# Kernel optimization log

Hardware: AMD Instinct MI355X
Metric: run time of the kernel (lower is better)

Reference implementation:

```python
import jax, jax.numpy as jnp
import numpy as np

B, NP, N, C, H = 16, 512, 1024, 1024, 16
HD = C // H
HID = 4 * C
EPS = 1e-5


def _layernorm(x, g, b):
    mu = jnp.mean(x, axis=-1, keepdims=True)
    var = jnp.mean(jnp.square(x - mu), axis=-1, keepdims=True)
    return (x - mu) * jax.lax.rsqrt(var + EPS) * g + b


def setup_inputs() -> dict:
    key = jax.random.key(0)
    ks = jax.random.split(key, 12)
    x = jax.random.normal(ks[0], (B, NP, C), dtype=jnp.float32)
    cache_k = jax.random.normal(ks[1], (B, H, N, HD), dtype=jnp.float32)
    cache_v = jax.random.normal(ks[2], (B, H, N, HD), dtype=jnp.float32)
    # update_mask: exactly NP active (to-be-updated) token slots per batch row
    scores = jax.random.uniform(ks[3], (B, N))
    top = jnp.argsort(scores, axis=1)[:, :NP]
    update_mask = jnp.zeros((B, N), dtype=bool).at[jnp.arange(B)[:, None], top].set(True)
    s = 0.02
    qkv_w = jax.random.normal(ks[4], (C, 3 * C), dtype=jnp.float32) * s
    qkv_b = jnp.zeros((3 * C,), dtype=jnp.float32)
    proj_w = jax.random.normal(ks[5], (C, C), dtype=jnp.float32) * s
    proj_b = jnp.zeros((C,), dtype=jnp.float32)
    n1_g = jnp.ones((C,), dtype=jnp.float32)
    n1_b = jnp.zeros((C,), dtype=jnp.float32)
    n2_g = jnp.ones((C,), dtype=jnp.float32)
    n2_b = jnp.zeros((C,), dtype=jnp.float32)
    fc1_w = jax.random.normal(ks[6], (C, HID), dtype=jnp.float32) * s
    fc1_b = jnp.zeros((HID,), dtype=jnp.float32)
    fc2_w = jax.random.normal(ks[7], (HID, C), dtype=jnp.float32) * s
    fc2_b = jnp.zeros((C,), dtype=jnp.float32)
    return dict(x=x, cache_k=cache_k, cache_v=cache_v, update_mask=update_mask,
                qkv_w=qkv_w, qkv_b=qkv_b, proj_w=proj_w, proj_b=proj_b,
                n1_g=n1_g, n1_b=n1_b, n2_g=n2_g, n2_b=n2_b,
                fc1_w=fc1_w, fc1_b=fc1_b, fc2_w=fc2_w, fc2_b=fc2_b)


def reference(x, cache_k, cache_v, update_mask, qkv_w, qkv_b, proj_w, proj_b,
              n1_g, n1_b, n2_g, n2_b, fc1_w, fc1_b, fc2_w, fc2_b):
    Bq, Np, Cd = x.shape
    h = _layernorm(x, n1_g, n1_b)
    qkv = (h @ qkv_w + qkv_b).reshape(Bq, Np, 3, H, HD)
    q, k, v = jnp.moveaxis(qkv, 2, 0)               # each [B, Np, H, HD]
    q = jnp.swapaxes(q, 1, 2)                       # [B, H, Np, HD]
    k = jnp.swapaxes(k, 1, 2)
    v = jnp.swapaxes(v, 1, 2)
    # masked_scatter_: i-th new token -> i-th masked slot (row-uniform mask count)
    idx = jnp.argsort(jnp.logical_not(update_mask), axis=1)[:, :Np]  # [B, Np]
    k_full = jax.vmap(lambda c, i, kn: c.at[:, i, :].set(kn))(cache_k, idx, k)
    v_full = jax.vmap(lambda c, i, vn: c.at[:, i, :].set(vn))(cache_v, idx, v)
    scale = HD ** -0.5
    attn = jnp.einsum('bhqd,bhkd->bhqk', q * scale, k_full)  # [B,H,Np,N]
    attn = jax.nn.softmax(attn, axis=-1)
    o = jnp.einsum('bhqk,bhkd->bhqd', attn, v_full)
    o = jnp.swapaxes(o, 1, 2).reshape(Bq, Np, Cd)
    o = o @ proj_w + proj_b
    x = x + o
    h2 = _layernorm(x, n2_g, n2_b)
    mlp = jax.nn.gelu(h2 @ fc1_w + fc1_b, approximate=False) @ fc2_w + fc2_b
    return x + mlp
```

## Files before the change

kernel.cpp:

```cpp
#include <hip/hip_runtime.h>
#include <hip/hip_bf16.h>
#include <math.h>

#define Bd   16
#define NPd  512
#define Nd   1024
#define Cd   1024
#define Hd   16
#define HDd  64
#define HIDd 4096
#define EPSd 1e-5f
#define MRd  (Bd * NPd)

typedef unsigned short u16;
typedef __bf16 bf16x8 __attribute__((ext_vector_type(8)));
typedef float  f32x4  __attribute__((ext_vector_type(4)));

__device__ __forceinline__ u16 f2bf(float f) {
    unsigned int u = __builtin_bit_cast(unsigned int, f);
    u = u + 0x7fffu + ((u >> 16) & 1u);
    return (u16)(u >> 16);
}

__device__ __forceinline__ void async_load16(const void* g, void* l) {
    __builtin_amdgcn_global_load_lds(
        (const __attribute__((address_space(1))) void*)(uintptr_t)g,
        (__attribute__((address_space(3))) void*)(unsigned int)(uintptr_t)l,
        16, 0, 0);
}

__global__ __launch_bounds__(256) void build_src(const void* __restrict__ mask_raw,
                                                 int* __restrict__ src) {
    const int b = blockIdx.x;
    const int t = threadIdx.x;
    const unsigned char* m8 = (const unsigned char*)mask_raw;
    const int* m32 = (const int*)mask_raw;

    int c = 0;
    #pragma unroll
    for (int i = 0; i < 4; i++) c += (m8[b * Nd + t * 4 + i] != 0) ? 1 : 0;
    #pragma unroll
    for (int off = 1; off < 64; off <<= 1) c += __shfl_xor(c, off);
    __shared__ int warr[4];
    if ((t & 63) == 0) warr[t >> 6] = c;
    __syncthreads();
    const int c8 = warr[0] + warr[1] + warr[2] + warr[3];
    const bool use8 = (c8 == NPd);

    int f[4];
    #pragma unroll
    for (int i = 0; i < 4; i++) {
        const int n = t * 4 + i;
        f[i] = use8 ? (m8[b * Nd + n] != 0) : (m32[b * Nd + n] != 0);
    }
    const int loc = f[0] + f[1] + f[2] + f[3];

    int sc_ = loc;
    #pragma unroll
    for (int off = 1; off < 64; off <<= 1) {
        const int u = __shfl_up(sc_, off);
        if ((t & 63) >= off) sc_ += u;
    }
    __shared__ int wtot[4];
    __syncthreads();
    if ((t & 63) == 63) wtot[t >> 6] = sc_;
    __syncthreads();
    int base = 0;
    for (int w = 0; w < (t >> 6); w++) base += wtot[w];

    int run = base + sc_ - loc;
    #pragma unroll
    for (int i = 0; i < 4; i++) {
        const int n = t * 4 + i;
        src[b * Nd + n] = f[i] ? run : -1;
        run += f[i];
    }
}

__global__ __launch_bounds__(256) void ln_kernel(const float* __restrict__ x,
                                                 const float* __restrict__ g,
                                                 const float* __restrict__ bb,
                                                 u16* __restrict__ out) {
    const int row = blockIdx.x;
    const int t = threadIdx.x;
    const float* xr = x + (size_t)row * Cd;
    const float4 v = *(const float4*)(xr + t * 4);
    float s = v.x + v.y + v.z + v.w;
    float q = v.x * v.x + v.y * v.y + v.z * v.z + v.w * v.w;
    #pragma unroll
    for (int off = 1; off < 64; off <<= 1) {
        s += __shfl_xor(s, off);
        q += __shfl_xor(q, off);
    }
    __shared__ float ss[4], qq[4];
    if ((t & 63) == 0) { ss[t >> 6] = s; qq[t >> 6] = q; }
    __syncthreads();
    s = ss[0] + ss[1] + ss[2] + ss[3];
    q = qq[0] + qq[1] + qq[2] + qq[3];
    const float mu = s * (1.0f / Cd);
    const float var = q * (1.0f / Cd) - mu * mu;
    const float rs = rsqrtf(var + EPSd);
    const float4 gv = *(const float4*)(g + t * 4);
    const float4 bv = *(const float4*)(bb + t * 4);
    ushort4 r;
    r.x = f2bf((v.x - mu) * rs * gv.x + bv.x);
    r.y = f2bf((v.y - mu) * rs * gv.y + bv.y);
    r.z = f2bf((v.z - mu) * rs * gv.z + bv.z);
    r.w = f2bf((v.w - mu) * rs * gv.w + bv.w);
    *(ushort4*)(out + (size_t)row * Cd + t * 4) = r;
}

__global__ __launch_bounds__(256) void conv_t(const float* __restrict__ W,
                                              u16* __restrict__ Wt,
                                              int K, int N) {
    __shared__ float tile[32][33];
    const int k0 = blockIdx.y * 32;
    const int n0 = blockIdx.x * 32;
    const int t = threadIdx.x;
    const int row = t >> 3, c4 = (t & 7) * 4;
    const float4 v = *(const float4*)(W + (size_t)(k0 + row) * N + n0 + c4);
    tile[row][c4 + 0] = v.x;
    tile[row][c4 + 1] = v.y;
    tile[row][c4 + 2] = v.z;
    tile[row][c4 + 3] = v.w;
    __syncthreads();
    ushort4 o;
    o.x = f2bf(tile[c4 + 0][row]);
    o.y = f2bf(tile[c4 + 1][row]);
    o.z = f2bf(tile[c4 + 2][row]);
    o.w = f2bf(tile[c4 + 3][row]);
    *(ushort4*)(Wt + (size_t)(n0 + row) * K + k0 + c4) = o;
}

template <int EPI, typename OUT_T>
__global__ __launch_bounds__(256) void gemm_mfma(const u16* __restrict__ A,
                                                 const u16* __restrict__ Wt,
                                                 const float* __restrict__ bias,
                                                 const float* __restrict__ res,
                                                 OUT_T* __restrict__ out,
                                                 int K, int Nn) {
    __shared__ u16 As[2][128 * 32];
    __shared__ u16 Bs[2][128 * 32];

    const int t = threadIdx.x;
    const int L = t & 63;
    const int w = t >> 6;
    const int wm = w >> 1, wn = w & 1;

    const int gx = gridDim.x;
    const int nwg = gx * gridDim.y;
    int id = blockIdx.y * gx + blockIdx.x;
    id = (id & 7) * (nwg >> 3) + (id >> 3);
    const int m0 = (id / gx) * 128;
    const int n0 = (id % gx) * 128;

    const int srow = 32 * w + (L >> 2);
    const int scol = (L & 3) * 8;
    const u16* ap0 = A  + (size_t)(m0 + srow) * K + scol;
    const u16* ap1 = ap0 + (size_t)16 * K;
    const u16* bp0 = Wt + (size_t)(n0 + srow) * K + scol;
    const u16* bp1 = bp0 + (size_t)16 * K;

    f32x4 acc[4][4];
    const f32x4 zero = {0.f, 0.f, 0.f, 0.f};
    #pragma unroll
    for (int i = 0; i < 4; i++)
        #pragma unroll
        for (int j = 0; j < 4; j++) acc[i][j] = zero;

    const int frag_off = (L & 15) * 32 + (L >> 4) * 8;
    const int nsteps = K >> 5;

    async_load16(ap0, &As[0][w * 1024]);
    async_load16(ap1, &As[0][w * 1024 + 512]);
    async_load16(bp0, &Bs[0][w * 1024]);
    async_load16(bp1, &Bs[0][w * 1024 + 512]);
    __syncthreads();

    int cur = 0;
    for (int kt = 0; kt < nsteps; kt++) {
        const int nxt = cur ^ 1;
        if (kt + 1 < nsteps) {
            const int off = (kt + 1) << 5;
            async_load16(ap0 + off, &As[nxt][w * 1024]);
            async_load16(ap1 + off, &As[nxt][w * 1024 + 512]);
            async_load16(bp0 + off, &Bs[nxt][w * 1024]);
            async_load16(bp1 + off, &Bs[nxt][w * 1024 + 512]);
        }

        bf16x8 a[4], b[4];
        #pragma unroll
        for (int i = 0; i < 4; i++) {
            a[i] = *(const bf16x8*)&As[cur][(wm * 64 + i * 16) * 32 + frag_off];
            b[i] = *(const bf16x8*)&Bs[cur][(wn * 64 + i * 16) * 32 + frag_off];
        }
        #pragma unroll
        for (int i = 0; i < 4; i++)
            #pragma unroll
            for (int j = 0; j < 4; j++)
                acc[i][j] = __builtin_amdgcn_mfma_f32_16x16x32_bf16(a[i], b[j], acc[i][j], 0, 0, 0);

        __syncthreads();
        cur = nxt;
    }

    const int cn = n0 + wn * 64 + (L & 15);
    const int cm = m0 + wm * 64 + (L >> 4) * 4;
    #pragma unroll
    for (int i = 0; i < 4; i++) {
        #pragma unroll
        for (int j = 0; j < 4; j++) {
            const int nn = cn + j * 16;
            const float bv = bias[nn];
            #pragma unroll
            for (int r = 0; r < 4; r++) {
                const int mm = cm + i * 16 + r;
                float v = acc[i][j][r] + bv;
                if (EPI == 2) v = 0.5f * v * (1.0f + erff(v * 0.70710678118654752f));
                if (EPI == 1) v += res[(size_t)mm * Nn + nn];
                if constexpr (sizeof(OUT_T) == 2) out[(size_t)mm * Nn + nn] = (OUT_T)f2bf(v);
                else out[(size_t)mm * Nn + nn] = v;
            }
        }
    }
}

__global__ __launch_bounds__(256) void kv_cast(const u16* __restrict__ qkv,
                                               const float* __restrict__ ck,
                                               const float* __restrict__ cv,
                                               const int* __restrict__ srcArr,
                                               u16* __restrict__ Kb,
                                               u16* __restrict__ Vtb) {
    const int id = blockIdx.x;
    const int nt = id & 15, hh = (id >> 4) & 15, b = id >> 8;
    const int t = threadIdx.x;
    __shared__ u16 Vl[64][72];

    const int row = t >> 2;
    const int dd = (t & 3) * 16;
    const int n = nt * 64 + row;
    const int sidx = srcArr[b * Nd + n];

    u16 kv16[16], vv16[16];
    if (sidx >= 0) {
        const u16* kp = qkv + (size_t)(b * NPd + sidx) * 3072 + Cd + hh * 64 + dd;
        const u16* vp = kp + Cd;
        *(ulonglong2*)&kv16[0] = *(const ulonglong2*)kp;
        *(ulonglong2*)&kv16[8] = *(const ulonglong2*)(kp + 8);
        *(ulonglong2*)&vv16[0] = *(const ulonglong2*)vp;
        *(ulonglong2*)&vv16[8] = *(const ulonglong2*)(vp + 8);
    } else {
        const float* kp = ck + ((size_t)((b * Hd + hh) * Nd + n)) * HDd + dd;
        const float* vp = cv + ((size_t)((b * Hd + hh) * Nd + n)) * HDd + dd;
        #pragma unroll
        for (int c = 0; c < 4; c++) {
            const float4 kc4 = *(const float4*)(kp + c * 4);
            const float4 vc4 = *(const float4*)(vp + c * 4);
            kv16[c * 4 + 0] = f2bf(kc4.x); kv16[c * 4 + 1] = f2bf(kc4.y);
            kv16[c * 4 + 2] = f2bf(kc4.z); kv16[c * 4 + 3] = f2bf(kc4.w);
            vv16[c * 4 + 0] = f2bf(vc4.x); vv16[c * 4 + 1] = f2bf(vc4.y);
            vv16[c * 4 + 2] = f2bf(vc4.z); vv16[c * 4 + 3] = f2bf(vc4.w);
        }
    }

    u16* ko = Kb + ((size_t)((b * Hd + hh) * Nd + n)) * HDd + dd;
    *(ulonglong2*)ko = *(ulonglong2*)&kv16[0];
    *(ulonglong2*)(ko + 8) = *(ulonglong2*)&kv16[8];

    #pragma unroll
    for (int i = 0; i < 16; i++) Vl[row][dd + i] = vv16[i];
    __syncthreads();

    const int d = t >> 2, nc = (t & 3) * 16;
    u16 ov[16];
    #pragma unroll
    for (int i = 0; i < 16; i++) ov[i] = Vl[nc + i][d];
    u16* vo = Vtb + ((size_t)((b * Hd + hh) * HDd + d)) * Nd + nt * 64 + nc;
    *(ulonglong2*)vo = *(ulonglong2*)&ov[0];
    *(ulonglong2*)(vo + 8) = *(ulonglong2*)&ov[8];
}

__global__ __launch_bounds__(256) void attn_mfma(const u16* __restrict__ qkv,
                                                 const u16* __restrict__ Kb,
                                                 const u16* __restrict__ Vtb,
                                                 u16* __restrict__ attno) {
    const int orig = blockIdx.y * 256 + blockIdx.x;
    const int xc = orig & 7, pos = orig >> 3;
    const int bh = (xc << 5) | (pos >> 3);
    const int qt = pos & 7;
    const int b = bh >> 4, hh = bh & 15;
    const int t = threadIdx.x;
    const int L = t & 63;
    const int w = t >> 6;

    __shared__ u16 Qs[4096];
    __shared__ u16 Ks[4096];
    __shared__ u16 Vs[4096];
    __shared__ u16 Ps[4][16 * 72];

    const size_t kbase = (size_t)((b * Hd + hh) * Nd) * HDd;
    const size_t vbase = (size_t)((b * Hd + hh) * HDd) * Nd;

    #pragma unroll
    for (int j = 0; j < 2; j++) {
        const int row = 16 * w + 8 * j + (L >> 3);
        const int ch = (L & 7) ^ (row & 7);
        const u16* g = qkv + (size_t)(b * NPd + qt * 64 + row) * 3072 + hh * 64 + ch * 8;
        async_load16(g, Qs + (16 * w + 8 * j) * 64);
    }

    f32x4 acc[4];
    const f32x4 zero = {0.f, 0.f, 0.f, 0.f};
    #pragma unroll
    for (int nb = 0; nb < 4; nb++) acc[nb] = zero;
    float m_run[4] = {-INFINITY, -INFINITY, -INFINITY, -INFINITY};
    float l_run[4] = {0.f, 0.f, 0.f, 0.f};

    for (int kt = 0; kt < 16; kt++) {
        __syncthreads();
        #pragma unroll
        for (int j = 0; j < 2; j++) {
            const int row = 16 * w + 8 * j + (L >> 3);
            const int ch = (L & 7) ^ (row & 7);
            async_load16(Kb + kbase + (size_t)(kt * 64 + row) * 64 + ch * 8,
                         Ks + (16 * w + 8 * j) * 64);
            async_load16(Vtb + vbase + (size_t)row * Nd + kt * 64 + ch * 8,
                         Vs + (16 * w + 8 * j) * 64);
        }
        __syncthreads();

        const int qrow = 16 * w + (L & 15);
        const bf16x8 aq0 = *(const bf16x8*)&Qs[qrow * 64 + (((L >> 4)     ^ (L & 7)) * 8)];
        const bf16x8 aq1 = *(const bf16x8*)&Qs[qrow * 64 + (((4 + (L >> 4)) ^ (L & 7)) * 8)];

        f32x4 s[4];
        #pragma unroll
        for (int kb = 0; kb < 4; kb++) {
            const int krow = kb * 16 + (L & 15);
            const bf16x8 bk0 = *(const bf16x8*)&Ks[krow * 64 + (((L >> 4)     ^ (L & 7)) * 8)];
            const bf16x8 bk1 = *(const bf16x8*)&Ks[krow * 64 + (((4 + (L >> 4)) ^ (L & 7)) * 8)];
            s[kb] = __builtin_amdgcn_mfma_f32_16x16x32_bf16(aq0, bk0, zero, 0, 0, 0);
            s[kb] = __builtin_amdgcn_mfma_f32_16x16x32_bf16(aq1, bk1, s[kb], 0, 0, 0);
        }

        float al[4];
        float pb[4][4];
        #pragma unroll
        for (int r = 0; r < 4; r++) {
            float m = fmaxf(fmaxf(s[0][r], s[1][r]), fmaxf(s[2][r], s[3][r])) * 0.125f;
            m = fmaxf(m, __shfl_xor(m, 1));
            m = fmaxf(m, __shfl_xor(m, 2));
            m = fmaxf(m, __shfl_xor(m, 4));
            m = fmaxf(m, __shfl_xor(m, 8));
            const float mn = fmaxf(m_run[r], m);
            al[r] = __expf(m_run[r] - mn);
            m_run[r] = mn;
        }
        float ps[4] = {0.f, 0.f, 0.f, 0.f};
        #pragma unroll
        for (int kb = 0; kb < 4; kb++)
            #pragma unroll
            for (int r = 0; r < 4; r++) {
                const float p = __expf(s[kb][r] * 0.125f - m_run[r]);
                pb[kb][r] = p;
                ps[r] += p;
            }
        #pragma unroll
        for (int r = 0; r < 4; r++) {
            ps[r] += __shfl_xor(ps[r], 1);
            ps[r] += __shfl_xor(ps[r], 2);
            ps[r] += __shfl_xor(ps[r], 4);
            ps[r] += __shfl_xor(ps[r], 8);
            l_run[r] = l_run[r] * al[r] + ps[r];
        }
        #pragma unroll
        for (int nb = 0; nb < 4; nb++)
            #pragma unroll
            for (int r = 0; r < 4; r++) acc[nb][r] *= al[r];

        u16* pw = &Ps[w][0];
        #pragma unroll
        for (int kb = 0; kb < 4; kb++)
            #pragma unroll
            for (int r = 0; r < 4; r++)
                pw[((L >> 4) * 4 + r) * 72 + kb * 16 + (L & 15)] = f2bf(pb[kb][r]);

        const bf16x8 ap0 = *(const bf16x8*)&Ps[w][(L & 15) * 72 +      (L >> 4) * 8];
        const bf16x8 ap1 = *(const bf16x8*)&Ps[w][(L & 15) * 72 + 32 + (L >> 4) * 8];
        #pragma unroll
        for (int nb = 0; nb < 4; nb++) {
            const int drow = nb * 16 + (L & 15);
            const bf16x8 bv0 = *(const bf16x8*)&Vs[drow * 64 + (((L >> 4)     ^ (L & 7)) * 8)];
            const bf16x8 bv1 = *(const bf16x8*)&Vs[drow * 64 + (((4 + (L >> 4)) ^ (L & 7)) * 8)];
            acc[nb] = __builtin_amdgcn_mfma_f32_16x16x32_bf16(ap0, bv0, acc[nb], 0, 0, 0);
            acc[nb] = __builtin_amdgcn_mfma_f32_16x16x32_bf16(ap1, bv1, acc[nb], 0, 0, 0);
        }
    }

    float inv[4];
    #pragma unroll
    for (int r = 0; r < 4; r++) inv[r] = 1.0f / l_run[r];
    #pragma unroll
    for (int nb = 0; nb < 4; nb++)
        #pragma unroll
        for (int r = 0; r < 4; r++) {
            const int q = qt * 64 + w * 16 + (L >> 4) * 4 + r;
            const int d = nb * 16 + (L & 15);
            attno[(size_t)(b * NPd + q) * Cd + hh * 64 + d] = f2bf(acc[nb][r] * inv[r]);
        }
}

extern "C" void kernel_launch(void* const* d_in, const int* in_sizes, int n_in,
                              void* d_out, int out_size, void* d_ws, size_t ws_size,
                              hipStream_t stream) {
    const float* x       = (const float*)d_in[0];
    const float* cache_k = (const float*)d_in[1];
    const float* cache_v = (const float*)d_in[2];
    const void*  mask    = d_in[3];
    const float* qkv_w   = (const float*)d_in[4];
    const float* qkv_b   = (const float*)d_in[5];
    const float* proj_w  = (const float*)d_in[6];
    const float* proj_b  = (const float*)d_in[7];
    const float* n1_g    = (const float*)d_in[8];
    const float* n1_b    = (const float*)d_in[9];
    const float* n2_g    = (const float*)d_in[10];
    const float* n2_b    = (const float*)d_in[11];
    const float* fc1_w   = (const float*)d_in[12];
    const float* fc1_b   = (const float*)d_in[13];
    const float* fc2_w   = (const float*)d_in[14];
    const float* fc2_b   = (const float*)d_in[15];
    float* out = (float*)d_out;

    const size_t MR = (size_t)Bd * NPd;
    char* ws = (char*)d_ws;
    int*   srcArr = (int*)ws;
    float* x2     = (float*)(ws + 65536);
    u16*   h      = (u16*)(x2 + MR * Cd);
    u16*   attno  = h + MR * Cd;
    u16*   qkv    = attno + MR * Cd;
    u16*   Kb     = qkv + MR * 3 * Cd;
    u16*   Vtb    = Kb + (size_t)Bd * Hd * Nd * HDd;
    u16*   m1     = qkv;
    u16*   qkv_wt = Vtb + (size_t)Bd * Hd * Nd * HDd;
    u16*   proj_wt= qkv_wt + (size_t)3 * Cd * Cd;
    u16*   fc1_wt = proj_wt + (size_t)Cd * Cd;
    u16*   fc2_wt = fc1_wt + (size_t)Cd * HIDd;

    build_src<<<Bd, 256, 0, stream>>>(mask, srcArr);
    conv_t<<<dim3(3 * Cd / 32, Cd / 32),  256, 0, stream>>>(qkv_w,  qkv_wt,  Cd,   3 * Cd);
    conv_t<<<dim3(Cd / 32, Cd / 32),      256, 0, stream>>>(proj_w, proj_wt, Cd,   Cd);
    conv_t<<<dim3(HIDd / 32, Cd / 32),    256, 0, stream>>>(fc1_w,  fc1_wt,  Cd,   HIDd);
    conv_t<<<dim3(Cd / 32, HIDd / 32),    256, 0, stream>>>(fc2_w,  fc2_wt,  HIDd, Cd);

    ln_kernel<<<MR, 256, 0, stream>>>(x, n1_g, n1_b, h);
    gemm_mfma<0, u16><<<dim3(3 * Cd / 128, MR / 128), 256, 0, stream>>>(
        h, qkv_wt, qkv_b, nullptr, qkv, Cd, 3 * Cd);
    kv_cast<<<Bd * Hd * (Nd / 64), 256, 0, stream>>>(qkv, cache_k, cache_v, srcArr, Kb, Vtb);
    attn_mfma<<<dim3(Bd * Hd, NPd / 64), 256, 0, stream>>>(qkv, Kb, Vtb, attno);
    gemm_mfma<1, float><<<dim3(Cd / 128, MR / 128), 256, 0, stream>>>(
        attno, proj_wt, proj_b, x, x2, Cd, Cd);
    ln_kernel<<<MR, 256, 0, stream>>>(x2, n2_g, n2_b, h);
    gemm_mfma<2, u16><<<dim3(HIDd / 128, MR / 128), 256, 0, stream>>>(
        h, fc1_wt, fc1_b, nullptr, m1, Cd, HIDd);
    gemm_mfma<1, float><<<dim3(Cd / 128, MR / 128), 256, 0, stream>>>(
        m1, fc2_wt, fc2_b, x2, out, HIDd, Cd);
}
```

Before: 681.1 us.

## Triple-buffer GEMM LDS tiles and XOR-swizzle the shared layout

Moves the bf16 MFMA GEMM from double to triple buffering of LDS tiles. Global-to-LDS loads are issued two k-steps ahead, and explicit vmcnt waits plus a raw s_barrier replace the plain __syncthreads. It also XOR-swizzles the 16-byte column chunks in both the async store and the fragment reads to cut LDS bank conflicts. This uses 50% more shared memory, which may lower occupancy, and depends on the hand-counted vmcnt values being correct.

```diff
diff --git a/kernel.cpp b/kernel.cpp
--- a/kernel.cpp
+++ b/kernel.cpp
@@ -139,8 +139,8 @@
                                                  const float* __restrict__ res,
                                                  OUT_T* __restrict__ out,
                                                  int K, int Nn) {
-    __shared__ u16 As[2][128 * 32];
-    __shared__ u16 Bs[2][128 * 32];
+    __shared__ u16 As[3][128 * 32];
+    __shared__ u16 Bs[3][128 * 32];
 
     const int t = threadIdx.x;
     const int L = t & 63;
@@ -155,7 +155,7 @@
     const int n0 = (id % gx) * 128;
 
     const int srow = 32 * w + (L >> 2);
-    const int scol = (L & 3) * 8;
+    const int scol = (((L & 3) ^ ((L >> 3) & 3)) * 8);
     const u16* ap0 = A  + (size_t)(m0 + srow) * K + scol;
     const u16* ap1 = ap0 + (size_t)16 * K;
     const u16* bp0 = Wt + (size_t)(n0 + srow) * K + scol;
@@ -168,24 +168,28 @@
         #pragma unroll
         for (int j = 0; j < 4; j++) acc[i][j] = zero;
 
-    const int frag_off = (L & 15) * 32 + (L >> 4) * 8;
+    const int rr = L & 15;
+    const int frag_off = rr * 32 + ((((L >> 4)) ^ ((rr >> 1) & 3)) * 8);
     const int nsteps = K >> 5;
 
-    async_load16(ap0, &As[0][w * 1024]);
-    async_load16(ap1, &As[0][w * 1024 + 512]);
-    async_load16(bp0, &Bs[0][w * 1024]);
-    async_load16(bp1, &Bs[0][w * 1024 + 512]);
-    __syncthreads();
+#define STAGE_G(s_, kt_) do {                                   \
+        const int off_ = (kt_) << 5;                            \
+        async_load16(ap0 + off_, &As[s_][w * 1024]);            \
+        async_load16(ap1 + off_, &As[s_][w * 1024 + 512]);      \
+        async_load16(bp0 + off_, &Bs[s_][w * 1024]);            \
+        async_load16(bp1 + off_, &Bs[s_][w * 1024 + 512]);      \
+    } while (0)
+
+    STAGE_G(0, 0);
+    STAGE_G(1, 1);
+    asm volatile("s_waitcnt vmcnt(4)" ::: "memory");
+    __builtin_amdgcn_s_barrier();
 
     int cur = 0;
     for (int kt = 0; kt < nsteps; kt++) {
-        const int nxt = cur ^ 1;
-        if (kt + 1 < nsteps) {
-            const int off = (kt + 1) << 5;
-            async_load16(ap0 + off, &As[nxt][w * 1024]);
-            async_load16(ap1 + off, &As[nxt][w * 1024 + 512]);
-            async_load16(bp0 + off, &Bs[nxt][w * 1024]);
-            async_load16(bp1 + off, &Bs[nxt][w * 1024 + 512]);
+        if (kt + 2 < nsteps) {
+            int s2 = cur + 2; if (s2 >= 3) s2 -= 3;
+            STAGE_G(s2, kt + 2);
         }
 
         bf16x8 a[4], b[4];
@@ -200,9 +204,12 @@
             for (int j = 0; j < 4; j++)
                 acc[i][j] = __builtin_amdgcn_mfma_f32_16x16x32_bf16(a[i], b[j], acc[i][j], 0, 0, 0);
 
-        __syncthreads();
-        cur = nxt;
-    }
+        if (kt + 2 < nsteps) asm volatile("s_waitcnt vmcnt(4)" ::: "memory");
+        else                 asm volatile("s_waitcnt vmcnt(0)" ::: "memory");
+        __builtin_amdgcn_s_barrier();
+        cur = (cur + 1 == 3) ? 0 : cur + 1;
+    }
+#undef STAGE_G
 
     const int cn = n0 + wn * 64 + (L & 15);
     const int cm = m0 + wm * 64 + (L >> 4) * 4;
```

Result: faster. 637.2 us (-6.4%).
